# Optimization experiments

Hardware: AMD Instinct MI355X
Metric: run time of the kernel (lower is better)

The kernel has to match this reference:

```python
import jax, jax.numpy as jnp
import numpy as np

B = 256          # graphs per batch
NC, NP = 16384, 131072   # compound / protein node counts
EC, EP = 131072, 2097152 # edge counts
D = 128


def _gconv(x, src, dst, W, b, n):
    # DGL GraphConv, norm='both': h = D_in^{-1/2} A D_out^{-1/2} x W + b
    ones = jnp.ones(src.shape, x.dtype)
    out_deg = jax.ops.segment_sum(ones, src, num_segments=n)
    in_deg = jax.ops.segment_sum(ones, dst, num_segments=n)
    ns = jax.lax.rsqrt(jnp.maximum(out_deg, 1.0))
    nd = jax.lax.rsqrt(jnp.maximum(in_deg, 1.0))
    h = (x * ns[:, None]) @ W           # apply weight before aggregation (same math, less traffic)
    m = jax.ops.segment_sum(h[src], dst, num_segments=n)  # SpMM aggregation
    return m * nd[:, None] + b


def _mean_nodes(x, gid, nb):
    s = jax.ops.segment_sum(x, gid, num_segments=nb)
    cnt = jax.ops.segment_sum(jnp.ones((x.shape[0],), x.dtype), gid, num_segments=nb)
    return s / jnp.maximum(cnt, 1.0)[:, None]


def setup_inputs() -> dict:
    key = jax.random.key(0)
    ks = jax.random.split(key, 24)
    s = 0.05
    inp = {
        "compound_feat": jax.random.normal(ks[0], (NC, 74), jnp.float32),
        "protein_feat": jax.random.normal(ks[1], (NP, 128), jnp.float32),
        # graph structure
        "c_src": jax.random.randint(ks[2], (EC,), 0, NC, jnp.int32),
        "c_dst": jax.random.randint(ks[3], (EC,), 0, NC, jnp.int32),
        "p_src": jax.random.randint(ks[4], (EP,), 0, NP, jnp.int32),
        "p_dst": jax.random.randint(ks[5], (EP,), 0, NP, jnp.int32),
        "c_gid": jax.random.randint(ks[6], (NC,), 0, B, jnp.int32),
        "p_gid": jax.random.randint(ks[7], (NP,), 0, B, jnp.int32),
        # GraphConv params
        "Wc1": jax.random.normal(ks[8], (74, D), jnp.float32) * s,
        "bc1": jnp.zeros((D,), jnp.float32),
        "Wc2": jax.random.normal(ks[9], (D, D), jnp.float32) * s,
        "bc2": jnp.zeros((D,), jnp.float32),
        "Wp1": jax.random.normal(ks[10], (128, D), jnp.float32) * s,
        "bp1": jnp.zeros((D,), jnp.float32),
        "Wp2": jax.random.normal(ks[11], (D, D), jnp.float32) * s,
        "bp2": jnp.zeros((D,), jnp.float32),
        # predictor MLP
        "Wf1": jax.random.normal(ks[12], (2 * D, D), jnp.float32) * s,
        "bf1": jnp.zeros((D,), jnp.float32),
        "Wf2": jax.random.normal(ks[13], (D, 1), jnp.float32) * s,
        "bf2": jnp.zeros((1,), jnp.float32),
    }
    return inp


def reference(compound_feat, protein_feat, c_src, c_dst, p_src, p_dst, c_gid, p_gid,
              Wc1, bc1, Wc2, bc2, Wp1, bp1, Wp2, bp2, Wf1, bf1, Wf2, bf2):
    c = jax.nn.relu(_gconv(compound_feat, c_src, c_dst, Wc1, bc1, NC))
    c = jax.nn.relu(_gconv(c, c_src, c_dst, Wc2, bc2, NC))
    c_global = _mean_nodes(c, c_gid, B)                     # [B, D]
    p = jax.nn.relu(_gconv(protein_feat, p_src, p_dst, Wp1, bp1, NP))
    p = jax.nn.relu(_gconv(p, p_src, p_dst, Wp2, bp2, NP))
    p_global = _mean_nodes(p, p_gid, B)                     # [B, D]
    combined = jnp.concatenate([c_global, p_global], axis=1)  # [B, 2D]
    h = jax.nn.relu(combined @ Wf1 + bf1)
    out = h @ Wf2 + bf2                                     # [B, 1]
    return out.squeeze(-1)
```

## Files before the change

### kernel.cpp

```cpp
#include <hip/hip_runtime.h>
#include <hip/hip_fp16.h>

#define D 128
#define SCH 4096
#define NBLK 256

typedef _Float16 half8 __attribute__((ext_vector_type(8)));
typedef float f32x4 __attribute__((ext_vector_type(4)));

struct HTask { const int* keys; int n; int shift; int* H; };
struct H6 { HTask t[6]; };

struct SPTask { const int* in; int n; int* part; };
struct SP6 { SPTask t[6]; };

struct SDTask { const int* in; int n; const int* part; int* out; int* total; };
struct SD6 { SDTask t[6]; };

struct ScTask { const int* k1; const int* k2; int n; int shift;
                const int* base1; const int* base2;
                int* o1; int* o2k; int* o2v; int mode; };
struct Sc4 { ScTask t[4]; };

struct CTask { const int* tmpk; const int* base; int n; int fine; int* deg; };
struct C4 { CTask t[4]; };

struct NTask { const int* outdeg; const int* indeg; float* ns; float* nd; int n; };
struct N2 { NTask t[2]; };

struct LTask { const int* tmpk; const int* tmpv; const int* base; int n;
               const int* rowptr; int shift; int fine; int* col; };
struct L2T { LTask t[2]; };

struct WPk { const float* W; _Float16* out; int K; };
struct W4 { WPk t[4]; };

struct GTask { const float* x; const float* ns; const _Float16* Wp; __half* h; int K; };
struct GemP { GTask t[2]; int nb0; };

struct ATask { const __half* h; const int* rowptr; const int* col;
               const float* nd; const float* b; void* out; int halfOut; };
struct AggP { ATask t[2]; int np; int ntot; };

struct MTask { const __half* x; const int* gbase; int n; const int* list; float* out; };
struct M2 { MTask t[2]; };


__global__ __launch_bounds__(256) void k_hist_all(H6 P) {
  HTask tk = P.t[blockIdx.y];
  __shared__ int bins[256];
  int blk = blockIdx.x, t = threadIdx.x;
  bins[t] = 0;
  __syncthreads();
  int per = (tk.n + NBLK - 1) / NBLK;
  int beg = blk * per, end = min(beg + per, tk.n);
  for (int i = beg + t; i < end; i += 256)
    atomicAdd(&bins[tk.keys[i] >> tk.shift], 1);
  __syncthreads();
  tk.H[t * NBLK + blk] = bins[t];
}

__global__ __launch_bounds__(256) void k_scan_part_all(SP6 P) {
  SPTask tk = P.t[blockIdx.y];
  int b = blockIdx.x, t = threadIdx.x;
  int base = b * SCH;
  int s = 0;
  for (int i = t; i < SCH; i += 256) {
    int idx = base + i;
    if (idx < tk.n) s += tk.in[idx];
  }
  __shared__ int red[256];
  red[t] = s;
  __syncthreads();
  for (int d = 128; d > 0; d >>= 1) {
    if (t < d) red[t] += red[t + d];
    __syncthreads();
  }
  if (t == 0) tk.part[b] = red[0];
}

__global__ __launch_bounds__(256) void k_scan_down_all(SD6 P) {
  SDTask tk = P.t[blockIdx.y];
  int b = blockIdx.x, t = threadIdx.x;
  int lane = t & 63, wid = t >> 6;
  __shared__ int wsum[4];
  if (b == 0 && t == 0 && tk.total) {
    int s = 0;
    for (int w = 0; w < (int)gridDim.x; ++w) s += tk.part[w];
    *tk.total = s;
  }
  int offset = 0;
  for (int w = 0; w < b; ++w) offset += tk.part[w];
  int base = b * SCH;
  if (base >= tk.n) return;
  int idx0 = base + t * 16;
  int v[16];
  int s = 0;
#pragma unroll
  for (int i = 0; i < 16; ++i) {
    int idx = idx0 + i;
    v[i] = (idx < tk.n) ? tk.in[idx] : 0;
    s += v[i];
  }
  int inc = s;
  for (int d = 1; d < 64; d <<= 1) {
    int u = __shfl_up(inc, d, 64);
    if (lane >= d) inc += u;
  }
  if (lane == 63) wsum[wid] = inc;
  __syncthreads();
  int woff = 0;
  for (int w = 0; w < wid; ++w) woff += wsum[w];
  int ex = offset + woff + inc - s;
#pragma unroll
  for (int i = 0; i < 16; ++i) {
    int idx = idx0 + i;
    if (idx < tk.n) tk.out[idx] = ex;
    ex += v[i];
  }
}

__global__ __launch_bounds__(256) void k_scatter_all(Sc4 P) {
  ScTask tk = P.t[blockIdx.y];
  __shared__ int curA[256], curB[256];
  int blk = blockIdx.x, t = threadIdx.x;
  curA[t] = tk.base1[t * NBLK + blk];
  if (tk.mode == 0) curB[t] = tk.base2[t * NBLK + blk];
  __syncthreads();
  int per = (tk.n + NBLK - 1) / NBLK;
  int beg = blk * per, end = min(beg + per, tk.n);
  if (tk.mode == 0) {
    for (int i = beg + t; i < end; i += 256) {
      int s = tk.k1[i], d = tk.k2[i];
      int pa = atomicAdd(&curA[s >> tk.shift], 1);
      tk.o1[pa] = s;
      int pb = atomicAdd(&curB[d >> tk.shift], 1);
      tk.o2k[pb] = d;
      tk.o2v[pb] = s;
    }
  } else {
    for (int i = beg + t; i < end; i += 256) {
      int pa = atomicAdd(&curA[tk.k1[i] >> tk.shift], 1);
      tk.o1[pa] = i;
    }
  }
}

__global__ __launch_bounds__(256) void k_l2count_all(C4 P) {
  CTask tk = P.t[blockIdx.y];
  __shared__ int bins[512];
  int b = blockIdx.x, t = threadIdx.x;
  for (int f = t; f < tk.fine; f += 256) bins[f] = 0;
  __syncthreads();
  int beg = tk.base[b * NBLK];
  int end = (b == NBLK - 1) ? tk.n : tk.base[(b + 1) * NBLK];
  for (int i = beg + t; i < end; i += 256)
    atomicAdd(&bins[tk.tmpk[i] & (tk.fine - 1)], 1);
  __syncthreads();
  for (int f = t; f < tk.fine; f += 256)
    tk.deg[b * tk.fine + f] = bins[f];
}

__global__ __launch_bounds__(256) void k_norms_all(N2 P) {
  NTask tk = P.t[blockIdx.y];
  int i = blockIdx.x * blockDim.x + threadIdx.x;
  if (i < tk.n) {
    tk.ns[i] = rsqrtf(fmaxf((float)tk.outdeg[i], 1.f));
    tk.nd[i] = rsqrtf(fmaxf((float)tk.indeg[i], 1.f));
  }
}

__global__ __launch_bounds__(256) void k_l2scatter_all(L2T P) {
  LTask tk = P.t[blockIdx.y];
  __shared__ int cur[512];
  int b = blockIdx.x, t = threadIdx.x;
  int v0 = b << tk.shift;
  for (int f = t; f < tk.fine; f += 256) cur[f] = tk.rowptr[v0 + f];
  __syncthreads();
  int beg = tk.base[b * NBLK];
  int end = (b == NBLK - 1) ? tk.n : tk.base[(b + 1) * NBLK];
  for (int i = beg + t; i < end; i += 256) {
    int pos = atomicAdd(&cur[tk.tmpk[i] & (tk.fine - 1)], 1);
    tk.col[pos] = tk.tmpv[i];
  }
}


__global__ __launch_bounds__(256) void k_wpack(W4 P) {
  WPk tk = P.t[blockIdx.y];
  int f = blockIdx.x;
  int kch = (tk.K + 31) >> 5;
  if (f >= (kch << 3)) return;
  int kc = f >> 3, nt = f & 7;
  int t = threadIdx.x;
  int l = t & 63, e0 = (t >> 6) << 1;
  int col = (nt << 4) + (l & 15);
  int kb = (kc << 5) + ((l >> 4) << 3);
#pragma unroll
  for (int e = e0; e < e0 + 2; ++e) {
    int k = kb + e;
    float v = (k < tk.K) ? tk.W[(size_t)k * D + col] : 0.f;
    tk.out[(((size_t)f * 64 + l) << 3) + e] = (_Float16)v;
  }
}

__global__ __launch_bounds__(256) void k_nl_gemm(GemP P) {
  __shared__ __align__(16) _Float16 Bs[32 * 64 * 8];
  int bx = blockIdx.x;
  GTask tk;
  int v0;
  if (bx < P.nb0) { tk = P.t[0]; v0 = bx * 128; }
  else            { tk = P.t[1]; v0 = (bx - P.nb0) * 128; }
  const int K = tk.K;
  const int kch = (K + 31) >> 5;
  int t = threadIdx.x, w = t >> 6, l = t & 63;

  {
    const uint4* src = (const uint4*)tk.Wp;
    uint4* dst = (uint4*)Bs;
    int n16 = kch << 9;
    for (int i = t; i < n16; i += 256) dst[i] = src[i];
  }
  __syncthreads();

  int row = l & 15;
  int ks = (l >> 4) << 3;
  int m0 = v0 + (w << 5);
  const float* x0 = tk.x + (size_t)(m0 + row) * K + ks;
  const float* x1 = tk.x + (size_t)(m0 + 16 + row) * K + ks;

  f32x4 acc[2][8];
  f32x4 zero = {0.f, 0.f, 0.f, 0.f};
#pragma unroll
  for (int i = 0; i < 2; ++i)
#pragma unroll
    for (int j = 0; j < 8; ++j) acc[i][j] = zero;

  for (int kc = 0; kc < kch; ++kc) {
    half8 a0, a1;
    if (K == D) {
      float4 p0 = *(const float4*)(x0 + (kc << 5));
      float4 p1 = *(const float4*)(x0 + (kc << 5) + 4);
      float4 q0 = *(const float4*)(x1 + (kc << 5));
      float4 q1 = *(const float4*)(x1 + (kc << 5) + 4);
      a0[0] = (_Float16)p0.x; a0[1] = (_Float16)p0.y;
      a0[2] = (_Float16)p0.z; a0[3] = (_Float16)p0.w;
      a0[4] = (_Float16)p1.x; a0[5] = (_Float16)p1.y;
      a0[6] = (_Float16)p1.z; a0[7] = (_Float16)p1.w;
      a1[0] = (_Float16)q0.x; a1[1] = (_Float16)q0.y;
      a1[2] = (_Float16)q0.z; a1[3] = (_Float16)q0.w;
      a1[4] = (_Float16)q1.x; a1[5] = (_Float16)q1.y;
      a1[6] = (_Float16)q1.z; a1[7] = (_Float16)q1.w;
    } else {
#pragma unroll
      for (int e = 0; e < 8; ++e) {
        int k = (kc << 5) + ks + e;
        a0[e] = (k < K) ? (_Float16)x0[(kc << 5) + e] : (_Float16)0.f;
        a1[e] = (k < K) ? (_Float16)x1[(kc << 5) + e] : (_Float16)0.f;
      }
    }
#pragma unroll
    for (int nt = 0; nt < 8; ++nt) {
      half8 b = *(const half8*)&Bs[(size_t)((((kc << 3) + nt) << 6) + l) << 3];
      acc[0][nt] = __builtin_amdgcn_mfma_f32_16x16x32_f16(a0, b, acc[0][nt], 0, 0, 0);
      acc[1][nt] = __builtin_amdgcn_mfma_f32_16x16x32_f16(a1, b, acc[1][nt], 0, 0, 0);
    }
  }

  int rr = (l >> 4) << 2;
  int c0 = l & 15;
#pragma unroll
  for (int mt = 0; mt < 2; ++mt) {
    int vb = m0 + (mt << 4) + rr;
    float s0 = tk.ns[vb], s1 = tk.ns[vb + 1];
    float s2 = tk.ns[vb + 2], s3 = tk.ns[vb + 3];
#pragma unroll
    for (int nt = 0; nt < 8; ++nt) {
      __half* hp = tk.h + (size_t)vb * D + (nt << 4) + c0;
      hp[0]     = __float2half_rn(acc[mt][nt][0] * s0);
      hp[D]     = __float2half_rn(acc[mt][nt][1] * s1);
      hp[2 * D] = __float2half_rn(acc[mt][nt][2] * s2);
      hp[3 * D] = __float2half_rn(acc[mt][nt][3] * s3);
    }
  }
}

__global__ __launch_bounds__(256) void k_aggregate(AggP P) {
  int wid = threadIdx.x >> 6;
  int lane = threadIdx.x & 63;
  int gv = blockIdx.x * 4 + wid;
  if (gv >= P.ntot) return;
  ATask tk;
  int v;
  if (gv < P.np) { tk = P.t[0]; v = gv; }
  else           { tk = P.t[1]; v = gv - P.np; }
  int beg = tk.rowptr[v], end = tk.rowptr[v + 1];
  int f0 = (lane & 15) * 8;
  int rsel = lane >> 4;
  const __half* h = tk.h;
  const int* col = tk.col;

  float acc[8];
#pragma unroll
  for (int k = 0; k < 8; ++k) acc[k] = 0.f;

  for (int j = beg; j < end; j += 8) {
    int j0 = j + rsel, j1 = j + 4 + rsel;
    if (j0 < end) {
      int c0 = col[j0];
      uint4 r = *(const uint4*)&h[(size_t)c0 * D + f0];
      const __half2* q = (const __half2*)&r;
#pragma unroll
      for (int k = 0; k < 4; ++k) {
        float2 f = __half22float2(q[k]);
        acc[2 * k] += f.x; acc[2 * k + 1] += f.y;
      }
    }
    if (j1 < end) {
      int c1 = col[j1];
      uint4 r = *(const uint4*)&h[(size_t)c1 * D + f0];
      const __half2* q = (const __half2*)&r;
#pragma unroll
      for (int k = 0; k < 4; ++k) {
        float2 f = __half22float2(q[k]);
        acc[2 * k] += f.x; acc[2 * k + 1] += f.y;
      }
    }
  }

#pragma unroll
  for (int k = 0; k < 8; ++k) {
    acc[k] += __shfl_down(acc[k], 32, 64);
    acc[k] += __shfl_down(acc[k], 16, 64);
  }

  if (rsel == 0) {
    float s = tk.nd[v];
    float4 b0 = *(const float4*)&tk.b[f0];
    float4 b1 = *(const float4*)&tk.b[f0 + 4];
    float r[8];
    r[0] = fmaxf(fmaf(acc[0], s, b0.x), 0.f);
    r[1] = fmaxf(fmaf(acc[1], s, b0.y), 0.f);
    r[2] = fmaxf(fmaf(acc[2], s, b0.z), 0.f);
    r[3] = fmaxf(fmaf(acc[3], s, b0.w), 0.f);
    r[4] = fmaxf(fmaf(acc[4], s, b1.x), 0.f);
    r[5] = fmaxf(fmaf(acc[5], s, b1.y), 0.f);
    r[6] = fmaxf(fmaf(acc[6], s, b1.z), 0.f);
    r[7] = fmaxf(fmaf(acc[7], s, b1.w), 0.f);
    if (tk.halfOut) {
      union { __half2 h2[4]; uint4 u; } pk;
#pragma unroll
      for (int k = 0; k < 4; ++k) {
        pk.h2[k].x = __float2half_rn(r[2 * k]);
        pk.h2[k].y = __float2half_rn(r[2 * k + 1]);
      }
      *(uint4*)&((__half*)tk.out)[(size_t)v * D + f0] = pk.u;
    } else {
      float4 o0 = {r[0], r[1], r[2], r[3]};
      float4 o1 = {r[4], r[5], r[6], r[7]};
      *(float4*)&((float*)tk.out)[(size_t)v * D + f0] = o0;
      *(float4*)&((float*)tk.out)[(size_t)v * D + f0 + 4] = o1;
    }
  }
}

__device__ __forceinline__ void acc_half4(float4& a, const __half* p) {
  uint2 r = *(const uint2*)p;
  __half2 q0 = *(__half2*)&r.x;
  __half2 q1 = *(__half2*)&r.y;
  float2 f0 = __half22float2(q0);
  float2 f1 = __half22float2(q1);
  a.x += f0.x; a.y += f0.y; a.z += f1.x; a.w += f1.y;
}

__global__ __launch_bounds__(256) void k_seg_mean(M2 P) {
  MTask tk = P.t[blockIdx.y];
  int g = blockIdx.x, t = threadIdx.x;
  int slot = t >> 5;
  int c = (t & 31) * 4;
  int beg = tk.gbase[g * NBLK];
  int end = (g == (int)gridDim.x - 1) ? tk.n : tk.gbase[(g + 1) * NBLK];
  const __half* x = tk.x;
  const int* list = tk.list;

  float4 a0 = make_float4(0.f, 0.f, 0.f, 0.f);
  float4 a1 = make_float4(0.f, 0.f, 0.f, 0.f);
  int j = beg + slot;
  for (; j + 8 < end; j += 16) {
    int s0 = list[j], s1 = list[j + 8];
    acc_half4(a0, x + (size_t)s0 * D + c);
    acc_half4(a1, x + (size_t)s1 * D + c);
  }
  if (j < end)
    acc_half4(a0, x + (size_t)list[j] * D + c);
  a0.x += a1.x; a0.y += a1.y; a0.z += a1.z; a0.w += a1.w;

  a0.x += __shfl_down(a0.x, 32, 64);
  a0.y += __shfl_down(a0.y, 32, 64);
  a0.z += __shfl_down(a0.z, 32, 64);
  a0.w += __shfl_down(a0.w, 32, 64);

  __shared__ float sred[4][32 * 4];
  int wid = t >> 6, lane = t & 63;
  if (lane < 32) *(float4*)&sred[wid][lane * 4] = a0;
  __syncthreads();
  if (t < 32) {
    float4 s0 = *(const float4*)&sred[0][t * 4];
    float4 s1 = *(const float4*)&sred[1][t * 4];
    float4 s2 = *(const float4*)&sred[2][t * 4];
    float4 s3 = *(const float4*)&sred[3][t * 4];
    float inv = 1.f / fmaxf((float)(end - beg), 1.f);
    float4 r;
    r.x = (s0.x + s1.x + s2.x + s3.x) * inv;
    r.y = (s0.y + s1.y + s2.y + s3.y) * inv;
    r.z = (s0.z + s1.z + s2.z + s3.z) * inv;
    r.w = (s0.w + s1.w + s2.w + s3.w) * inv;
    *(float4*)&tk.out[(size_t)g * D + c] = r;
  }
}

__global__ void k_mlp(const float* __restrict__ cg, const float* __restrict__ pg,
                      const float* __restrict__ Wf1, const float* __restrict__ bf1,
                      const float* __restrict__ Wf2, const float* __restrict__ bf2,
                      float* __restrict__ out) {
  __shared__ float xs[256];
  __shared__ float red[128];
  int b = blockIdx.x, t = threadIdx.x;
  xs[t] = cg[b * D + t];
  xs[128 + t] = pg[b * D + t];
  __syncthreads();
  float acc = bf1[t];
  for (int k = 0; k < 256; ++k) acc = fmaf(xs[k], Wf1[k * D + t], acc);
  float hv = fmaxf(acc, 0.f);
  red[t] = hv * Wf2[t];
  for (int d = 64; d > 0; d >>= 1) {
    __syncthreads();
    if (t < d) red[t] += red[t + d];
  }
  if (t == 0) out[b] = red[0] + bf2[0];
}


extern "C" void kernel_launch(void* const* d_in, const int* in_sizes, int n_in,
                              void* d_out, int out_size, void* d_ws, size_t ws_size,
                              hipStream_t stream) {
  const float* compound_feat = (const float*)d_in[0];
  const float* protein_feat  = (const float*)d_in[1];
  const int* c_src = (const int*)d_in[2];
  const int* c_dst = (const int*)d_in[3];
  const int* p_src = (const int*)d_in[4];
  const int* p_dst = (const int*)d_in[5];
  const int* c_gid = (const int*)d_in[6];
  const int* p_gid = (const int*)d_in[7];
  const float* Wc1 = (const float*)d_in[8];  const float* bc1 = (const float*)d_in[9];
  const float* Wc2 = (const float*)d_in[10]; const float* bc2 = (const float*)d_in[11];
  const float* Wp1 = (const float*)d_in[12]; const float* bp1 = (const float*)d_in[13];
  const float* Wp2 = (const float*)d_in[14]; const float* bp2 = (const float*)d_in[15];
  const float* Wf1 = (const float*)d_in[16]; const float* bf1 = (const float*)d_in[17];
  const float* Wf2 = (const float*)d_in[18]; const float* bf2 = (const float*)d_in[19];
  float* out = (float*)d_out;

  const int EC = in_sizes[2], EP = in_sizes[4];
  const int NC = in_sizes[6], NP = in_sizes[7];
  const int B  = out_size;
  const int KC = in_sizes[0] / NC;
  const int cshift = __builtin_ctz(NC / 256), cfine = NC / 256;
  const int pshift = __builtin_ctz(NP / 256), pfine = NP / 256;
  const int HN = 256 * NBLK;

  char* ws = (char*)d_ws;
  size_t off = 0;
  auto alloc = [&](size_t bytes) -> void* {
    void* p = ws + off;
    off += (bytes + 255) & ~(size_t)255;
    return p;
  };

  int* H0 = (int*)alloc((size_t)HN * 4);
  int* H1 = (int*)alloc((size_t)HN * 4);
  int* H2 = (int*)alloc((size_t)HN * 4);
  int* H3 = (int*)alloc((size_t)HN * 4);
  int* H4 = (int*)alloc((size_t)HN * 4);
  int* H5 = (int*)alloc((size_t)HN * 4);
  int* partH = (int*)alloc((size_t)6 * 32 * 4);
  int* partD = (int*)alloc((size_t)2 * 32 * 4);
  int* tmps_c = (int*)alloc((size_t)EC * 4);
  int* tmpd_c = (int*)alloc((size_t)EC * 4);
  int* tmpv_c = (int*)alloc((size_t)EC * 4);
  int* tmps_p = (int*)alloc((size_t)EP * 4);
  int* tmpd_p = (int*)alloc((size_t)EP * 4);
  int* tmpv_p = (int*)alloc((size_t)EP * 4);
  int* c_outdeg = (int*)alloc((size_t)NC * 4);
  int* c_indeg  = (int*)alloc((size_t)NC * 4);
  int* p_outdeg = (int*)alloc((size_t)NP * 4);
  int* p_indeg  = (int*)alloc((size_t)NP * 4);
  float* c_ns = (float*)alloc((size_t)NC * 4);
  float* c_nd = (float*)alloc((size_t)NC * 4);
  float* p_ns = (float*)alloc((size_t)NP * 4);
  float* p_nd = (float*)alloc((size_t)NP * 4);
  int* c_rowptr = (int*)alloc((size_t)(NC + 1) * 4);
  int* p_rowptr = (int*)alloc((size_t)(NP + 1) * 4);
  int* c_col   = (int*)alloc((size_t)EC * 4);
  int* p_col   = (int*)alloc((size_t)EP * 4);
  int* cg_list = (int*)alloc((size_t)NC * 4);
  int* pg_list = (int*)alloc((size_t)NP * 4);
  __half* c_h  = (__half*)alloc((size_t)NC * D * 2);
  float*  c_m1 = (float*) alloc((size_t)NC * D * 4);
  __half* c_m2 = (__half*)alloc((size_t)NC * D * 2);
  __half* p_h  = (__half*)alloc((size_t)NP * D * 2);
  float*  p_m1 = (float*) alloc((size_t)NP * D * 4);
  __half* p_m2 = (__half*)alloc((size_t)NP * D * 2);
  float* cg = (float*)alloc((size_t)B * D * 4);
  float* pg = (float*)alloc((size_t)B * D * 4);
  _Float16* wp_p1 = (_Float16*)alloc((size_t)32 * 1024);
  _Float16* wp_c1 = (_Float16*)alloc((size_t)32 * 1024);
  _Float16* wp_p2 = (_Float16*)alloc((size_t)32 * 1024);
  _Float16* wp_c2 = (_Float16*)alloc((size_t)32 * 1024);
  (void)ws_size; (void)n_in;

  {
    W4 PW = {{{Wp1, wp_p1, D}, {Wc1, wp_c1, KC}, {Wp2, wp_p2, D}, {Wc2, wp_c2, D}}};
    k_wpack<<<dim3(32, 4), 256, 0, stream>>>(PW);
  }
  {
    H6 P = {{{c_src, EC, cshift, H0}, {c_dst, EC, cshift, H1}, {c_gid, NC, 0, H2},
             {p_src, EP, pshift, H3}, {p_dst, EP, pshift, H4}, {p_gid, NP, 0, H5}}};
    k_hist_all<<<dim3(NBLK, 6), 256, 0, stream>>>(P);
  }
  {
    SP6 Pp = {{{H0, HN, partH + 0}, {H1, HN, partH + 32}, {H2, HN, partH + 64},
               {H3, HN, partH + 96}, {H4, HN, partH + 128}, {H5, HN, partH + 160}}};
    k_scan_part_all<<<dim3(16, 6), 256, 0, stream>>>(Pp);
    SD6 Pd = {{{H0, HN, partH + 0, H0, nullptr}, {H1, HN, partH + 32, H1, nullptr},
               {H2, HN, partH + 64, H2, nullptr}, {H3, HN, partH + 96, H3, nullptr},
               {H4, HN, partH + 128, H4, nullptr}, {H5, HN, partH + 160, H5, nullptr}}};
    k_scan_down_all<<<dim3(16, 6), 256, 0, stream>>>(Pd);
  }
  {
    Sc4 P = {{{c_src, c_dst, EC, cshift, H0, H1, tmps_c, tmpd_c, tmpv_c, 0},
              {p_src, p_dst, EP, pshift, H3, H4, tmps_p, tmpd_p, tmpv_p, 0},
              {c_gid, nullptr, NC, 0, H2, nullptr, cg_list, nullptr, nullptr, 1},
              {p_gid, nullptr, NP, 0, H5, nullptr, pg_list, nullptr, nullptr, 1}}};
    k_scatter_all<<<dim3(NBLK, 4), 256, 0, stream>>>(P);
  }
  {
    C4 P = {{{tmps_c, H0, EC, cfine, c_outdeg}, {tmpd_c, H1, EC, cfine, c_indeg},
             {tmps_p, H3, EP, pfine, p_outdeg}, {tmpd_p, H4, EP, pfine, p_indeg}}};
    k_l2count_all<<<dim3(NBLK, 4), 256, 0, stream>>>(P);
  }
  {
    SP6 Pp; Pp.t[0] = {c_indeg, NC, partD + 0}; Pp.t[1] = {p_indeg, NP, partD + 32};
    Pp.t[2] = Pp.t[3] = Pp.t[4] = Pp.t[5] = SPTask{c_indeg, 0, partD + 0};
    k_scan_part_all<<<dim3(32, 2), 256, 0, stream>>>(Pp);
    SD6 Pd; Pd.t[0] = {c_indeg, NC, partD + 0, c_rowptr, c_rowptr + NC};
    Pd.t[1] = {p_indeg, NP, partD + 32, p_rowptr, p_rowptr + NP};
    Pd.t[2] = Pd.t[3] = Pd.t[4] = Pd.t[5] = Pd.t[0];
    k_scan_down_all<<<dim3(32, 2), 256, 0, stream>>>(Pd);
  }
  {
    N2 P = {{{c_outdeg, c_indeg, c_ns, c_nd, NC}, {p_outdeg, p_indeg, p_ns, p_nd, NP}}};
    k_norms_all<<<dim3((NP + 255) / 256, 2), 256, 0, stream>>>(P);
  }
  {
    L2T P = {{{tmpd_c, tmpv_c, H1, EC, c_rowptr, cshift, cfine, c_col},
              {tmpd_p, tmpv_p, H4, EP, p_rowptr, pshift, pfine, p_col}}};
    k_l2scatter_all<<<dim3(NBLK, 2), 256, 0, stream>>>(P);
  }

  const int gnb = NP / 128 + NC / 128;
  const int anb = (NP + NC + 3) / 4;
  {
    GemP P = {{{protein_feat, p_ns, wp_p1, p_h, D}, {compound_feat, c_ns, wp_c1, c_h, KC}}, NP / 128};
    k_nl_gemm<<<gnb, 256, 0, stream>>>(P);
  }
  {
    AggP P = {{{p_h, p_rowptr, p_col, p_nd, bp1, p_m1, 0},
               {c_h, c_rowptr, c_col, c_nd, bc1, c_m1, 0}}, NP, NP + NC};
    k_aggregate<<<anb, 256, 0, stream>>>(P);
  }
  {
    GemP P = {{{p_m1, p_ns, wp_p2, p_h, D}, {c_m1, c_ns, wp_c2, c_h, D}}, NP / 128};
    k_nl_gemm<<<gnb, 256, 0, stream>>>(P);
  }
  {
    AggP P = {{{p_h, p_rowptr, p_col, p_nd, bp2, p_m2, 1},
               {c_h, c_rowptr, c_col, c_nd, bc2, c_m2, 1}}, NP, NP + NC};
    k_aggregate<<<anb, 256, 0, stream>>>(P);
  }
  {
    M2 P = {{{c_m2, H2, NC, cg_list, cg}, {p_m2, H5, NP, pg_list, pg}}};
    k_seg_mean<<<dim3(B, 2), 256, 0, stream>>>(P);
  }

  k_mlp<<<B, D, 0, stream>>>(cg, pg, Wf1, bf1, Wf2, bf2, out);
}
```

Baseline: 554.8 us.

## Store layer-1 aggregate in fp16 and batch column loads in aggregation

The first-layer aggregation now writes its output in half precision instead of fp32, and the second GEMM reads half8 vectors directly, cutting the intermediate write and read traffic in half and removing the conversions. The aggregation loop also processes 16 edges per iteration, loading four column indices before issuing the gathers, to expose more memory-level parallelism. The cost is extra rounding of the intermediate activations to fp16.

```diff
diff --git a/kernel.cpp b/kernel.cpp
--- a/kernel.cpp
+++ b/kernel.cpp
@@ -35,7 +35,8 @@
 struct WPk { const float* W; _Float16* out; int K; };
 struct W4 { WPk t[4]; };
 
-struct GTask { const float* x; const float* ns; const _Float16* Wp; __half* h; int K; };
+struct GTask { const void* x; const float* ns; const _Float16* Wp; __half* h;
+               int K; int xh; };
 struct GemP { GTask t[2]; int nb0; };
 
 struct ATask { const __half* h; const int* rowptr; const int* col;
@@ -226,8 +227,15 @@
   int row = l & 15;
   int ks = (l >> 4) << 3;
   int m0 = v0 + (w << 5);
-  const float* x0 = tk.x + (size_t)(m0 + row) * K + ks;
-  const float* x1 = tk.x + (size_t)(m0 + 16 + row) * K + ks;
+  const float* xf0 = nullptr; const float* xf1 = nullptr;
+  const _Float16* xh0 = nullptr; const _Float16* xh1 = nullptr;
+  if (tk.xh) {
+    xh0 = (const _Float16*)tk.x + (size_t)(m0 + row) * D + ks;
+    xh1 = xh0 + (size_t)16 * D;
+  } else {
+    xf0 = (const float*)tk.x + (size_t)(m0 + row) * K + ks;
+    xf1 = xf0 + (size_t)16 * K;
+  }
 
   f32x4 acc[2][8];
   f32x4 zero = {0.f, 0.f, 0.f, 0.f};
@@ -238,11 +246,14 @@
 
   for (int kc = 0; kc < kch; ++kc) {
     half8 a0, a1;
-    if (K == D) {
-      float4 p0 = *(const float4*)(x0 + (kc << 5));
-      float4 p1 = *(const float4*)(x0 + (kc << 5) + 4);
-      float4 q0 = *(const float4*)(x1 + (kc << 5));
-      float4 q1 = *(const float4*)(x1 + (kc << 5) + 4);
+    if (tk.xh) {
+      a0 = *(const half8*)(xh0 + (kc << 5));
+      a1 = *(const half8*)(xh1 + (kc << 5));
+    } else if (K == D) {
+      float4 p0 = *(const float4*)(xf0 + (kc << 5));
+      float4 p1 = *(const float4*)(xf0 + (kc << 5) + 4);
+      float4 q0 = *(const float4*)(xf1 + (kc << 5));
+      float4 q1 = *(const float4*)(xf1 + (kc << 5) + 4);
       a0[0] = (_Float16)p0.x; a0[1] = (_Float16)p0.y;
       a0[2] = (_Float16)p0.z; a0[3] = (_Float16)p0.w;
       a0[4] = (_Float16)p1.x; a0[5] = (_Float16)p1.y;
@@ -255,8 +266,8 @@
 #pragma unroll
       for (int e = 0; e < 8; ++e) {
         int k = (kc << 5) + ks + e;
-        a0[e] = (k < K) ? (_Float16)x0[(kc << 5) + e] : (_Float16)0.f;
-        a1[e] = (k < K) ? (_Float16)x1[(kc << 5) + e] : (_Float16)0.f;
+        a0[e] = (k < K) ? (_Float16)xf0[(kc << 5) + e] : (_Float16)0.f;
+        a1[e] = (k < K) ? (_Float16)xf1[(kc << 5) + e] : (_Float16)0.f;
       }
     }
 #pragma unroll
@@ -304,26 +315,24 @@
 #pragma unroll
   for (int k = 0; k < 8; ++k) acc[k] = 0.f;
 
-  for (int j = beg; j < end; j += 8) {
-    int j0 = j + rsel, j1 = j + 4 + rsel;
-    if (j0 < end) {
-      int c0 = col[j0];
-      uint4 r = *(const uint4*)&h[(size_t)c0 * D + f0];
-      const __half2* q = (const __half2*)&r;
-#pragma unroll
-      for (int k = 0; k < 4; ++k) {
-        float2 f = __half22float2(q[k]);
-        acc[2 * k] += f.x; acc[2 * k + 1] += f.y;
-      }
-    }
-    if (j1 < end) {
-      int c1 = col[j1];
-      uint4 r = *(const uint4*)&h[(size_t)c1 * D + f0];
-      const __half2* q = (const __half2*)&r;
-#pragma unroll
-      for (int k = 0; k < 4; ++k) {
-        float2 f = __half22float2(q[k]);
-        acc[2 * k] += f.x; acc[2 * k + 1] += f.y;
+  for (int j = beg; j < end; j += 16) {
+    int jj[4];
+    int cc[4];
+#pragma unroll
+    for (int q = 0; q < 4; ++q) {
+      jj[q] = j + 4 * q + rsel;
+      cc[q] = (jj[q] < end) ? col[jj[q]] : -1;
+    }
+#pragma unroll
+    for (int q = 0; q < 4; ++q) {
+      if (cc[q] >= 0) {
+        uint4 r = *(const uint4*)&h[(size_t)cc[q] * D + f0];
+        const __half2* p = (const __half2*)&r;
+#pragma unroll
+        for (int k = 0; k < 4; ++k) {
+          float2 f = __half22float2(p[k]);
+          acc[2 * k] += f.x; acc[2 * k + 1] += f.y;
+        }
       }
     }
   }
@@ -505,10 +514,10 @@
   int* cg_list = (int*)alloc((size_t)NC * 4);
   int* pg_list = (int*)alloc((size_t)NP * 4);
   __half* c_h  = (__half*)alloc((size_t)NC * D * 2);
-  float*  c_m1 = (float*) alloc((size_t)NC * D * 4);
+  __half* c_m1 = (__half*)alloc((size_t)NC * D * 2);
   __half* c_m2 = (__half*)alloc((size_t)NC * D * 2);
   __half* p_h  = (__half*)alloc((size_t)NP * D * 2);
-  float*  p_m1 = (float*) alloc((size_t)NP * D * 4);
+  __half* p_m1 = (__half*)alloc((size_t)NP * D * 2);
   __half* p_m2 = (__half*)alloc((size_t)NP * D * 2);
   float* cg = (float*)alloc((size_t)B * D * 4);
   float* pg = (float*)alloc((size_t)B * D * 4);
@@ -570,16 +579,17 @@
   const int gnb = NP / 128 + NC / 128;
   const int anb = (NP + NC + 3) / 4;
   {
-    GemP P = {{{protein_feat, p_ns, wp_p1, p_h, D}, {compound_feat, c_ns, wp_c1, c_h, KC}}, NP / 128};
+    GemP P = {{{protein_feat, p_ns, wp_p1, p_h, D, 0},
+               {compound_feat, c_ns, wp_c1, c_h, KC, 0}}, NP / 128};
     k_nl_gemm<<<gnb, 256, 0, stream>>>(P);
   }
   {
-    AggP P = {{{p_h, p_rowptr, p_col, p_nd, bp1, p_m1, 0},
-               {c_h, c_rowptr, c_col, c_nd, bc1, c_m1, 0}}, NP, NP + NC};
+    AggP P = {{{p_h, p_rowptr, p_col, p_nd, bp1, p_m1, 1},
+               {c_h, c_rowptr, c_col, c_nd, bc1, c_m1, 1}}, NP, NP + NC};
     k_aggregate<<<anb, 256, 0, stream>>>(P);
   }
   {
-    GemP P = {{{p_m1, p_ns, wp_p2, p_h, D}, {c_m1, c_ns, wp_c2, c_h, D}}, NP / 128};
+    GemP P = {{{p_m1, p_ns, wp_p2, p_h, D, 1}, {c_m1, c_ns, wp_c2, c_h, D, 1}}, NP / 128};
     k_nl_gemm<<<gnb, 256, 0, stream>>>(P);
   }
   {
```

New measurement: 528.1 us. 4.8% less time.
